# Optimization experiments

Measured on AMD Instinct MI355X. Metric: run time of the kernel, lower is better.

The kernel has to match this reference:

```python
import jax, jax.numpy as jnp
import numpy as np


def floor_ste(x):
    # forward: floor(x); backward: identity (straight-through estimator)
    return x + jax.lax.stop_gradient(jnp.floor(x) - x)


def _int_polynomial(x_int, sf):
    c0, c1, c2 = 0.35815147, 0.96963238, 1.0
    b_int = floor_ste((c1 / c0) / sf)
    c_int = floor_ste((c2 / c0) / (sf * sf))
    z = x_int * (x_int + b_int) + c_int
    return z, c0 * sf * sf


def _int_exp(x_int, sf):
    x0 = -0.69314718
    n = 15
    x0_int = floor_ste(x0 / sf)
    x_int = jnp.maximum(x_int, n * x0_int)
    q = floor_ste(x_int / x0_int)
    r = x_int - x0_int * q
    exp_int, exp_sf = _int_polynomial(r, sf)
    exp_int = jnp.maximum(floor_ste(exp_int * jnp.exp2(n - q)), 0.0)
    return exp_int, exp_sf / (2.0 ** n)


def _int_softmax(x, sf):
    x_int = x / sf
    x_int = x_int - jnp.max(x_int, axis=-1, keepdims=True)
    exp_int, exp_sf = _int_exp(x_int, sf)
    exp_int_sum = jnp.sum(exp_int, axis=-1, keepdims=True)
    return exp_int, exp_int_sum, exp_sf


def setup_inputs() -> dict:
    key = jax.random.key(0)
    k1, = jax.random.split(key, 1)
    x = jax.random.normal(k1, (2, 16, 1024, 1024), dtype=jnp.float32)
    scale = jnp.float32(0.05)          # activation quantization step
    threshold = jnp.array([0.1], dtype=jnp.float32)  # nn.Parameter init
    return {"x": x, "scale": scale, "threshold": threshold}


def reference(x, scale, threshold):
    output_bit = 8
    threshold_bits = 8
    exp_int, exp_int_sum, exp_sf = _int_softmax(x, scale)
    factor = floor_ste((2.0 ** 32) / exp_int_sum)
    out_scale_A = threshold / (2.0 ** output_bit - 1.0)   # shape [1]
    out_scale_B = 1.0 / (2.0 ** output_bit - 1.0)
    approx_threshold = (floor_ste(threshold * 2.0 ** threshold_bits)
                        * exp_int_sum / (2.0 ** threshold_bits))
    mask_A = exp_int <= approx_threshold
    exp_int_A = jnp.where(mask_A, exp_int, 0.0)
    exp_int_B = jnp.where(mask_A, 0.0, exp_int)
    softmax_int_A = floor_ste(exp_int_A * factor / ((2.0 ** 32) * out_scale_A))
    softmax_int_B = floor_ste(exp_int_B * factor / ((2.0 ** 32) * out_scale_B))
    softmax_int_B = jnp.minimum(softmax_int_B, 255.0)
    return softmax_int_A * out_scale_A + softmax_int_B * out_scale_B
```

## Files before the change

kernel.cpp:

```cpp
#include <hip/hip_runtime.h>
#include <math.h>

#pragma clang fp contract(off)

#define TPB 256
#define ROWLEN 1024

__global__ __launch_bounds__(TPB) void qsplit_int_softmax_kernel(
    const float* __restrict__ x,
    const float* __restrict__ scale_p,
    const float* __restrict__ thr_p,
    float* __restrict__ out)
{
    const int row = blockIdx.x;
    const int tid = threadIdx.x;
    const size_t base = (size_t)row * ROWLEN + (size_t)tid * 4;

    const float4 xv = *(const float4*)(x + base);

    const double sf  = (double)scale_p[0];
    const double thr = (double)thr_p[0];

    const double rsf    = 1.0 / sf;
    const double x0_int = floor(-0.69314718 / sf);
    const double b_int  = floor((0.96963238 / 0.35815147) / sf);
    const double c_int  = floor((1.0 / 0.35815147) / (sf * sf));
    const double clampv = 15.0 * x0_int;
    const double inv_x0 = 1.0 / x0_int;

    double xiv[4];
    xiv[0] = (double)xv.x * rsf;
    xiv[1] = (double)xv.y * rsf;
    xiv[2] = (double)xv.z * rsf;
    xiv[3] = (double)xv.w * rsf;

    double m = fmax(fmax(xiv[0], xiv[1]), fmax(xiv[2], xiv[3]));
    #pragma unroll
    for (int off = 1; off < 64; off <<= 1)
        m = fmax(m, __shfl_xor(m, off));

    __shared__ double sred[2][4];
    const int wave = tid >> 6;
    if ((tid & 63) == 0) sred[0][wave] = m;
    __syncthreads();
    m = fmax(fmax(sred[0][0], sred[0][1]), fmax(sred[0][2], sred[0][3]));

    double e[4];
    double lsum = 0.0;
    #pragma unroll
    for (int j = 0; j < 4; ++j) {
        double v = xiv[j] - m;
        v = fmax(v, clampv);
        int qi = (int)(v * inv_x0);
        if (qi > 15) qi = 15;
        double r = v - x0_int * (double)qi;
        double t = r + b_int;
        double z = r * t + c_int;
        double pw = (double)(1 << (15 - qi));
        double ei = floor(z * pw);
        ei = fmax(ei, 0.0);
        e[j] = ei;
        lsum += ei;
    }

    #pragma unroll
    for (int off = 1; off < 64; off <<= 1)
        lsum += __shfl_xor(lsum, off);
    if ((tid & 63) == 0) sred[1][wave] = lsum;
    __syncthreads();
    const double s = (sred[1][0] + sred[1][1]) + (sred[1][2] + sred[1][3]);

    const double factor = floor(4294967296.0 / s);
    const double osA  = thr / 255.0;
    const double osB  = 1.0 / 255.0;
    const double denA = 4294967296.0 * osA;
    const double denB = 4294967296.0 * osB;
    const double invDenA = 1.0 / denA;
    const double invDenB = 1.0 / denB;
    const double ath  = (floor(thr * 256.0) * s) * (1.0 / 256.0);

    float4 o;
    float res[4];
    #pragma unroll
    for (int j = 0; j < 4; ++j) {
        const double ei = e[j];
        const bool isA = (ei <= ath);
        const double numer = ei * factor;
        double sA = 0.0, sB = 0.0;
        if (isA) {
            sA = floor(numer * invDenA);
        } else {
            sB = fmin(floor(numer * invDenB), 255.0);
        }
        res[j] = (float)(sA * osA + sB * osB);
    }
    o.x = res[0]; o.y = res[1]; o.z = res[2]; o.w = res[3];
    *(float4*)(out + base) = o;
}

extern "C" void kernel_launch(void* const* d_in, const int* in_sizes, int n_in,
                              void* d_out, int out_size, void* d_ws, size_t ws_size,
                              hipStream_t stream) {
    const float* x     = (const float*)d_in[0];
    const float* scale = (const float*)d_in[1];
    const float* thr   = (const float*)d_in[2];
    float* out = (float*)d_out;

    const int total = in_sizes[0];
    const int rows  = total / ROWLEN;

    qsplit_int_softmax_kernel<<<dim3(rows), dim3(TPB), 0, stream>>>(
        x, scale, thr, out);
}
```

Baseline: 234.8 us.

## Map one wavefront per row and move elementwise math from fp64 to fp32

Each 64-lane wavefront now handles a full 1024-element row with 16 elements per lane, so both reductions become wave shuffles with no shared memory or __syncthreads, and the grid shrinks by four. Most per-element arithmetic (exp polynomial, floor, ldexp, quantization) now runs in fp32 instead of fp64, with double kept only for the sum, threshold comparison and the final reciprocal multiply. This cuts fp64 ALU cost and block-level sync, but may round differently from the fp64 reference in edge cases.

```diff
diff --git a/kernel.cpp b/kernel.cpp
--- a/kernel.cpp
+++ b/kernel.cpp
@@ -12,90 +12,94 @@
     const float* __restrict__ thr_p,
     float* __restrict__ out)
 {
-    const int row = blockIdx.x;
-    const int tid = threadIdx.x;
-    const size_t base = (size_t)row * ROWLEN + (size_t)tid * 4;
+    const int lane = threadIdx.x & 63;
+    const int wid  = threadIdx.x >> 6;
+    const int row  = blockIdx.x * 4 + wid;
+    const size_t rbase = (size_t)row * ROWLEN + (size_t)lane * 4;
 
-    const float4 xv = *(const float4*)(x + base);
+    const float  sf   = scale_p[0];
+    const float  thr  = thr_p[0];
+    const double sfd  = (double)sf;
+    const double rsfd = 1.0 / sfd;
 
-    const double sf  = (double)scale_p[0];
-    const double thr = (double)thr_p[0];
+    const double x0d    = floor(-0.69314718 / sfd);
+    const float  x0f    = (float)x0d;
+    const float  bfc    = (float)floor((0.96963238 / 0.35815147) / sfd);
+    const float  cfc    = (float)floor((1.0 / 0.35815147) / (sfd * sfd));
+    const float  clampf = (float)(15.0 * x0d);
+    const float  invx0f = 1.0f / x0f;
 
-    const double rsf    = 1.0 / sf;
-    const double x0_int = floor(-0.69314718 / sf);
-    const double b_int  = floor((0.96963238 / 0.35815147) / sf);
-    const double c_int  = floor((1.0 / 0.35815147) / (sf * sf));
-    const double clampv = 15.0 * x0_int;
-    const double inv_x0 = 1.0 / x0_int;
+    float4 xv[4];
+    #pragma unroll
+    for (int k = 0; k < 4; ++k)
+        xv[k] = *(const float4*)(x + rbase + (size_t)k * 256);
 
-    double xiv[4];
-    xiv[0] = (double)xv.x * rsf;
-    xiv[1] = (double)xv.y * rsf;
-    xiv[2] = (double)xv.z * rsf;
-    xiv[3] = (double)xv.w * rsf;
+    float xi[16];
+    #pragma unroll
+    for (int k = 0; k < 4; ++k) {
+        xi[k*4+0] = (float)((double)xv[k].x * rsfd);
+        xi[k*4+1] = (float)((double)xv[k].y * rsfd);
+        xi[k*4+2] = (float)((double)xv[k].z * rsfd);
+        xi[k*4+3] = (float)((double)xv[k].w * rsfd);
+    }
 
-    double m = fmax(fmax(xiv[0], xiv[1]), fmax(xiv[2], xiv[3]));
+    float m = xi[0];
+    #pragma unroll
+    for (int j = 1; j < 16; ++j) m = fmaxf(m, xi[j]);
     #pragma unroll
     for (int off = 1; off < 64; off <<= 1)
-        m = fmax(m, __shfl_xor(m, off));
+        m = fmaxf(m, __shfl_xor(m, off));
 
-    __shared__ double sred[2][4];
-    const int wave = tid >> 6;
-    if ((tid & 63) == 0) sred[0][wave] = m;
-    __syncthreads();
-    m = fmax(fmax(sred[0][0], sred[0][1]), fmax(sred[0][2], sred[0][3]));
-
-    double e[4];
+    float e[16];
     double lsum = 0.0;
     #pragma unroll
-    for (int j = 0; j < 4; ++j) {
-        double v = xiv[j] - m;
-        v = fmax(v, clampv);
-        int qi = (int)(v * inv_x0);
-        if (qi > 15) qi = 15;
-        double r = v - x0_int * (double)qi;
-        double t = r + b_int;
-        double z = r * t + c_int;
-        double pw = (double)(1 << (15 - qi));
-        double ei = floor(z * pw);
-        ei = fmax(ei, 0.0);
+    for (int j = 0; j < 16; ++j) {
+        float v = xi[j] - m;
+        v = fmaxf(v, clampf);
+        float qf = floorf(v * invx0f);
+        int   ki = 15 - (int)qf;
+        float r  = v - x0f * qf;
+        float t  = r + bfc;
+        float z  = r * t + cfc;
+        float ei = floorf(ldexpf(z, ki));
+        ei = fmaxf(ei, 0.0f);
         e[j] = ei;
-        lsum += ei;
+        lsum += (double)ei;
     }
 
     #pragma unroll
     for (int off = 1; off < 64; off <<= 1)
         lsum += __shfl_xor(lsum, off);
-    if ((tid & 63) == 0) sred[1][wave] = lsum;
-    __syncthreads();
-    const double s = (sred[1][0] + sred[1][1]) + (sred[1][2] + sred[1][3]);
+    const double s = lsum;
 
-    const double factor = floor(4294967296.0 / s);
-    const double osA  = thr / 255.0;
-    const double osB  = 1.0 / 255.0;
-    const double denA = 4294967296.0 * osA;
-    const double denB = 4294967296.0 * osB;
-    const double invDenA = 1.0 / denA;
-    const double invDenB = 1.0 / denB;
-    const double ath  = (floor(thr * 256.0) * s) * (1.0 / 256.0);
+    const double factor_d = floor(4294967296.0 / s);
+    const float  fac_f = (float)factor_d;
+    const double ath   = (floor((double)thr * 256.0) * s) * (1.0 / 256.0);
 
-    float4 o;
-    float res[4];
+    const float  osA  = thr / 255.0f;
+    const float  osB  = 1.0f / 255.0f;
+    const float  denA = 4294967296.0f * osA;
+    const float  denB = 4294967296.0f * osB;
+    const double invA = 1.0 / (double)denA;
+    const double invB = 1.0 / (double)denB;
+
     #pragma unroll
-    for (int j = 0; j < 4; ++j) {
-        const double ei = e[j];
-        const bool isA = (ei <= ath);
-        const double numer = ei * factor;
-        double sA = 0.0, sB = 0.0;
-        if (isA) {
-            sA = floor(numer * invDenA);
-        } else {
-            sB = fmin(floor(numer * invDenB), 255.0);
+    for (int k = 0; k < 4; ++k) {
+        float res[4];
+        #pragma unroll
+        for (int jj = 0; jj < 4; ++jj) {
+            const float ei  = e[k*4+jj];
+            const bool  isA = ((double)ei <= ath);
+            const float numer = ei * fac_f;
+            const double inv  = isA ? invA : invB;
+            const float  qf2  = (float)((double)numer * inv);
+            float si = floorf(qf2);
+            si = fminf(si, isA ? 3.0e38f : 255.0f);
+            res[jj] = si * (isA ? osA : osB);
         }
-        res[j] = (float)(sA * osA + sB * osB);
+        float4 o; o.x = res[0]; o.y = res[1]; o.z = res[2]; o.w = res[3];
+        *(float4*)(out + rbase + (size_t)k * 256) = o;
     }
-    o.x = res[0]; o.y = res[1]; o.z = res[2]; o.w = res[3];
-    *(float4*)(out + base) = o;
 }
 
 extern "C" void kernel_launch(void* const* d_in, const int* in_sizes, int n_in,
@@ -108,7 +112,8 @@
 
     const int total = in_sizes[0];
     const int rows  = total / ROWLEN;
+    const int blocks = rows / 4;
 
-    qsplit_int_softmax_kernel<<<dim3(rows), dim3(TPB), 0, stream>>>(
+    qsplit_int_softmax_kernel<<<dim3(blocks), dim3(TPB), 0, stream>>>(
         x, scale, thr, out);
 }
```

After: 231.6 us. No clear change (-1.3%).
